# Kernel tuning notes

Measured on AMD Instinct MI355X. Metric: run time of the kernel, lower is better.

## Reference

```python
import jax, jax.numpy as jnp
import numpy as np

# pywt 'db4' decomposition filters (8 taps)
DEC_LO = np.array([-0.010597401784997278, 0.032883011666982945, 0.030841381835986965,
                   -0.18703481171888114, -0.02798376941698385, 0.6308807679295904,
                   0.7148465705525415, 0.23037781330885523], dtype=np.float32)
DEC_HI = np.array([-0.23037781330885523, 0.7148465705525415, -0.6308807679295904,
                   -0.02798376941698385, 0.18703481171888114, 0.030841381835986965,
                   -0.032883011666982945, -0.010597401784997278], dtype=np.float32)
FLEN = 8


def _dwt_last_axis(x, kern):
    """Single-level DWT along the last axis, pywt 'symmetric' mode.
    Equivalent to: pad symmetric by FLEN-1, np.convolve(ext, filt, 'valid')[1::2].
    kern: [2, 1, FLEN] (already time-reversed filters -> cross-correlation == convolution).
    Returns (lo, hi) each of shape x.shape[:-1] + (floor((n+FLEN-1)/2),).
    """
    pad = [(0, 0)] * (x.ndim - 1) + [(FLEN - 1, FLEN - 1)]
    xp = jnp.pad(x, pad, mode='symmetric')[..., 1:]  # drop 1 -> stride-2 grid starts at offset 1
    lead = xp.shape[:-1]
    xr = xp.reshape(-1, 1, xp.shape[-1])             # [N, 1, Lp]
    y = jax.lax.conv_general_dilated(
        xr, kern, window_strides=(2,), padding='VALID',
        dimension_numbers=('NCH', 'OIH', 'NCH'))     # [N, 2, out]
    y = y.reshape(lead + (2, y.shape[-1]))
    return y[..., 0, :], y[..., 1, :]


def setup_inputs() -> dict:
    key = jax.random.key(0)
    x = jax.random.normal(key, (8, 32, 512, 512), dtype=jnp.float32)
    return {"x": x}


def reference(x):
    # Batched 2D db4 DWT (pywt.dwt2, mode='symmetric') over [B, C, H, W].
    kern = jnp.stack([jnp.asarray(DEC_LO)[::-1], jnp.asarray(DEC_HI)[::-1]])[:, None, :]  # [2,1,8]
    # filter along W (axis -1)
    a_w, d_w = _dwt_last_axis(x, kern)
    # filter along H (axis -2): swap H/W, filter last axis, swap back
    def along_h(t):
        lo, hi = _dwt_last_axis(jnp.swapaxes(t, -1, -2), kern)
        return jnp.swapaxes(lo, -1, -2), jnp.swapaxes(hi, -1, -2)
    LL, LH = along_h(a_w)   # LL = aa, LH = cH = 'da' (detail along H, approx along W)
    HL, HH = along_h(d_w)   # HL = cV = 'ad', HH = cD = 'dd'
    return jnp.stack([LL, LH, HL, HH])  # [4, B, C, Ho, Wo]
```

## Files before the change

### kernel.cpp

```cpp
#include <hip/hip_runtime.h>


namespace {

constexpr int N   = 512;
constexpr int HO  = 259;
constexpr int NBC = 256;
constexpr int TOH = 12;
constexpr int NS  = (HO + TOH - 1) / TOH;
constexpr int NCG = 65;

typedef float f4 __attribute__((ext_vector_type(4)));
typedef f4 __attribute__((aligned(4))) f4u;
typedef float f2 __attribute__((ext_vector_type(2)));
typedef f2 __attribute__((aligned(4))) f2u;

__device__ constexpr float GL[8] = {
     0.23037781330885523f,  0.7148465705525415f,   0.6308807679295904f,
    -0.02798376941698385f, -0.18703481171888114f,  0.030841381835986965f,
     0.032883011666982945f,-0.010597401784997278f};
__device__ constexpr float GH[8] = {
    -0.010597401784997278f,-0.032883011666982945f, 0.030841381835986965f,
     0.18703481171888114f, -0.02798376941698385f, -0.6308807679295904f,
     0.7148465705525415f,  -0.23037781330885523f};

__device__ constexpr int LMAP[14] = {5,4,3,2,1,0,0,1,2,3,4,5,6,7};
__device__ constexpr int RMAP[14] = {8,9,10,11,12,13,13,12,11,10,9,8,7,6};

__device__ __forceinline__ int ext_idx(int j) {
    int v = j - 7;
    v = (j < 7)     ? (6 - j)         : v;
    v = (j > N + 6) ? (2 * N + 6 - j) : v;
    return v;
}

__device__ __forceinline__ void hconv(const float* __restrict__ base, int mode,
                                      f4& lo, f4& hi) {
    const f4 a = *(const f4u*)(base);
    const f4 b = *(const f4u*)(base + 4);
    const f4 c = *(const f4u*)(base + 8);
    const f2 d = *(const f2u*)(base + 12);
    const float win[14] = {a.x,a.y,a.z,a.w, b.x,b.y,b.z,b.w,
                           c.x,c.y,c.z,c.w, d.x,d.y};
    float v[14];
    if (mode == 0) {
        #pragma unroll
        for (int f = 0; f < 14; ++f) v[f] = win[f];
    } else if (mode < 0) {
        #pragma unroll
        for (int f = 0; f < 14; ++f) v[f] = win[LMAP[f]];
    } else {
        #pragma unroll
        for (int f = 0; f < 14; ++f) v[f] = win[RMAP[f]];
    }
    #pragma unroll
    for (int o = 0; o < 4; ++o) {
        float l = 0.f, h = 0.f;
        #pragma unroll
        for (int k = 0; k < 8; ++k) {
            l = fmaf(v[2 * o + k], GL[k], l);
            h = fmaf(v[2 * o + k], GH[k], h);
        }
        lo[o] = l; hi[o] = h;
    }
}

__global__ __launch_bounds__(256)
void dwt2_db4_reg(const float* __restrict__ x, float* __restrict__ out) {
    const int id   = blockIdx.x * 256 + threadIdx.x;
    const int cg   = id % NCG;
    const int rest = id / NCG;
    const int st   = rest % NS;
    const int bc   = rest / NS;
    const int c0   = 4 * cg;
    const int g0   = 2 * c0 - 6;
    const int g0c  = min(max(g0, 0), N - 14);
    const int mode = (cg == 0) ? -1 : ((cg == NCG - 1) ? 1 : 0);
    const float* __restrict__ img = x + (size_t)bc * (N * N);
    const int eh0 = 2 * (st * TOH) + 1;

    f4 rlo[8], rhi[8];
    #pragma unroll
    for (int r = 0; r < 6; ++r)
        hconv(img + (size_t)ext_idx(eh0 + r) * N + g0c, mode, rlo[r], rhi[r]);

    const size_t sub = (size_t)NBC * HO * HO;
    float* __restrict__ obase = out + (size_t)bc * (HO * HO);

#define STEP(U) do {                                                          \
    const int uo_ = ob * 4 + (U);                                             \
    const int e_  = eh0 + 2 * uo_ + 6;                                        \
    hconv(img + (size_t)ext_idx(e_)     * N + g0c, mode,                      \
          rlo[(6 + 2 * (U)) & 7], rhi[(6 + 2 * (U)) & 7]);                    \
    hconv(img + (size_t)ext_idx(e_ + 1) * N + g0c, mode,                      \
          rlo[(7 + 2 * (U)) & 7], rhi[(7 + 2 * (U)) & 7]);                    \
    f4 ll = {0,0,0,0}, lh = {0,0,0,0}, hl = {0,0,0,0}, hh = {0,0,0,0};        \
    _Pragma("unroll")                                                         \
    for (int k = 0; k < 8; ++k) {                                             \
        const f4 a_ = rlo[(2 * (U) + k) & 7];                                 \
        const f4 d_ = rhi[(2 * (U) + k) & 7];                                 \
        const float gl = GL[k], gh = GH[k];                                   \
        ll.x = fmaf(a_.x, gl, ll.x); ll.y = fmaf(a_.y, gl, ll.y);             \
        ll.z = fmaf(a_.z, gl, ll.z); ll.w = fmaf(a_.w, gl, ll.w);             \
        lh.x = fmaf(a_.x, gh, lh.x); lh.y = fmaf(a_.y, gh, lh.y);             \
        lh.z = fmaf(a_.z, gh, lh.z); lh.w = fmaf(a_.w, gh, lh.w);             \
        hl.x = fmaf(d_.x, gl, hl.x); hl.y = fmaf(d_.y, gl, hl.y);             \
        hl.z = fmaf(d_.z, gl, hl.z); hl.w = fmaf(d_.w, gl, hl.w);             \
        hh.x = fmaf(d_.x, gh, hh.x); hh.y = fmaf(d_.y, gh, hh.y);             \
        hh.z = fmaf(d_.z, gh, hh.z); hh.w = fmaf(d_.w, gh, hh.w);             \
    }                                                                         \
    const int ho_ = st * TOH + uo_;                                           \
    if (ho_ < HO) {                                                           \
        const size_t p = (size_t)ho_ * HO + c0;                               \
        if (cg != NCG - 1) {                                                  \
            *(f4u*)(obase + p)           = ll;                                \
            *(f4u*)(obase + sub + p)     = lh;                                \
            *(f4u*)(obase + 2 * sub + p) = hl;                                \
            *(f4u*)(obase + 3 * sub + p) = hh;                                \
        } else {                                                              \
            _Pragma("unroll")                                                 \
            for (int o = 0; o < 3; ++o) {                                     \
                obase[p + o]           = ll[o];                               \
                obase[sub + p + o]     = lh[o];                               \
                obase[2 * sub + p + o] = hl[o];                               \
                obase[3 * sub + p + o] = hh[o];                               \
            }                                                                 \
        }                                                                     \
    }                                                                         \
} while (0)

    for (int ob = 0; ob < TOH / 4; ++ob) {
        STEP(0); STEP(1); STEP(2); STEP(3);
    }
#undef STEP
}

}

extern "C" void kernel_launch(void* const* d_in, const int* in_sizes, int n_in,
                              void* d_out, int out_size, void* d_ws, size_t ws_size,
                              hipStream_t stream) {
    const float* x = (const float*)d_in[0];
    float* out = (float*)d_out;
    const int items  = NBC * NS * NCG;
    const int blocks = items / 256;
    dwt2_db4_reg<<<blocks, 256, 0, stream>>>(x, out);
}
```

Before: 143.8 us.

## Halve per-thread column work and use aligned 16-byte horizontal window loads

Each thread now computes two output columns instead of four, doubling the thread count, and loads a 12-float window from a 16-byte-aligned base with aligned vector loads instead of an unaligned 14-float window. Boundary handling is expanded to four symmetric-extension modes for the first two and last two column groups. This aims to raise parallelism, lower register pressure and use aligned loads. In exchange, redundant horizontal reads grow and output stores shrink to 8 bytes.

```diff
diff --git a/kernel.cpp b/kernel.cpp
--- a/kernel.cpp
+++ b/kernel.cpp
@@ -7,11 +7,10 @@
 constexpr int HO  = 259;
 constexpr int NBC = 256;
 constexpr int TOH = 12;
-constexpr int NS  = (HO + TOH - 1) / TOH;
-constexpr int NCG = 65;
+constexpr int NS  = 22;
+constexpr int NCG = 130;
 
 typedef float f4 __attribute__((ext_vector_type(4)));
-typedef f4 __attribute__((aligned(4))) f4u;
 typedef float f2 __attribute__((ext_vector_type(2)));
 typedef f2 __attribute__((aligned(4))) f2u;
 
@@ -24,10 +23,13 @@
      0.18703481171888114f, -0.02798376941698385f, -0.6308807679295904f,
      0.7148465705525415f,  -0.23037781330885523f};
 
-__device__ constexpr int LMAP[14] = {5,4,3,2,1,0,0,1,2,3,4,5,6,7};
-__device__ constexpr int RMAP[14] = {8,9,10,11,12,13,13,12,11,10,9,8,7,6};
+__device__ constexpr int IMAP[10] = {2,3,4,5,6,7,8,9,10,11};
+__device__ constexpr int LM0[10] = {5,4,3,2,1,0,0,1,2,3};
+__device__ constexpr int LM1[10] = {1,0,0,1,2,3,4,5,6,7};
+__device__ constexpr int RM0[10] = {6,7,8,9,10,11,11,10,9,8};
+__device__ constexpr int RM1[10] = {10,11,11,10,9,8,7,6,5,4};
 
-__device__ __forceinline__ int ext_idx(int j) {
+__device__ __forceinline__ int ext_row(int j) {
     int v = j - 7;
     v = (j < 7)     ? (6 - j)         : v;
     v = (j > N + 6) ? (2 * N + 6 - j) : v;
@@ -35,26 +37,36 @@
 }
 
 __device__ __forceinline__ void hconv(const float* __restrict__ base, int mode,
-                                      f4& lo, f4& hi) {
-    const f4 a = *(const f4u*)(base);
-    const f4 b = *(const f4u*)(base + 4);
-    const f4 c = *(const f4u*)(base + 8);
-    const f2 d = *(const f2u*)(base + 12);
-    const float win[14] = {a.x,a.y,a.z,a.w, b.x,b.y,b.z,b.w,
-                           c.x,c.y,c.z,c.w, d.x,d.y};
-    float v[14];
-    if (mode == 0) {
+                                      f2& lo, f2& hi) {
+    const f4 a = *(const f4*)(base);
+    const f4 b = *(const f4*)(base + 4);
+    const f4 c = *(const f4*)(base + 8);
+    const float win[12] = {a.x,a.y,a.z,a.w, b.x,b.y,b.z,b.w, c.x,c.y,c.z,c.w};
+    float v[10];
+    switch (mode) {
+    case 0:
         #pragma unroll
-        for (int f = 0; f < 14; ++f) v[f] = win[f];
-    } else if (mode < 0) {
+        for (int f = 0; f < 10; ++f) v[f] = win[IMAP[f]];
+        break;
+    case 1:
         #pragma unroll
-        for (int f = 0; f < 14; ++f) v[f] = win[LMAP[f]];
-    } else {
+        for (int f = 0; f < 10; ++f) v[f] = win[LM0[f]];
+        break;
+    case 2:
         #pragma unroll
-        for (int f = 0; f < 14; ++f) v[f] = win[RMAP[f]];
+        for (int f = 0; f < 10; ++f) v[f] = win[LM1[f]];
+        break;
+    case 3:
+        #pragma unroll
+        for (int f = 0; f < 10; ++f) v[f] = win[RM0[f]];
+        break;
+    default:
+        #pragma unroll
+        for (int f = 0; f < 10; ++f) v[f] = win[RM1[f]];
+        break;
     }
     #pragma unroll
-    for (int o = 0; o < 4; ++o) {
+    for (int o = 0; o < 2; ++o) {
         float l = 0.f, h = 0.f;
         #pragma unroll
         for (int k = 0; k < 8; ++k) {
@@ -66,23 +78,23 @@
 }
 
 __global__ __launch_bounds__(256)
-void dwt2_db4_reg(const float* __restrict__ x, float* __restrict__ out) {
+void dwt2_db4_reg2(const float* __restrict__ x, float* __restrict__ out) {
     const int id   = blockIdx.x * 256 + threadIdx.x;
     const int cg   = id % NCG;
     const int rest = id / NCG;
     const int st   = rest % NS;
     const int bc   = rest / NS;
-    const int c0   = 4 * cg;
-    const int g0   = 2 * c0 - 6;
-    const int g0c  = min(max(g0, 0), N - 14);
-    const int mode = (cg == 0) ? -1 : ((cg == NCG - 1) ? 1 : 0);
+    const int c0   = 2 * cg;
+    const int gb   = min(max(4 * cg - 8, 0), N - 12);
+    const int mode = (cg == 0) ? 1 : (cg == 1) ? 2 :
+                     (cg == NCG - 2) ? 3 : (cg == NCG - 1) ? 4 : 0;
     const float* __restrict__ img = x + (size_t)bc * (N * N);
     const int eh0 = 2 * (st * TOH) + 1;
 
-    f4 rlo[8], rhi[8];
+    f2 rlo[8], rhi[8];
     #pragma unroll
     for (int r = 0; r < 6; ++r)
-        hconv(img + (size_t)ext_idx(eh0 + r) * N + g0c, mode, rlo[r], rhi[r]);
+        hconv(img + (size_t)ext_row(eh0 + r) * N + gb, mode, rlo[r], rhi[r]);
 
     const size_t sub = (size_t)NBC * HO * HO;
     float* __restrict__ obase = out + (size_t)bc * (HO * HO);
@@ -90,41 +102,34 @@
 #define STEP(U) do {                                                          \
     const int uo_ = ob * 4 + (U);                                             \
     const int e_  = eh0 + 2 * uo_ + 6;                                        \
-    hconv(img + (size_t)ext_idx(e_)     * N + g0c, mode,                      \
+    hconv(img + (size_t)ext_row(e_)     * N + gb, mode,                       \
           rlo[(6 + 2 * (U)) & 7], rhi[(6 + 2 * (U)) & 7]);                    \
-    hconv(img + (size_t)ext_idx(e_ + 1) * N + g0c, mode,                      \
+    hconv(img + (size_t)ext_row(e_ + 1) * N + gb, mode,                       \
           rlo[(7 + 2 * (U)) & 7], rhi[(7 + 2 * (U)) & 7]);                    \
-    f4 ll = {0,0,0,0}, lh = {0,0,0,0}, hl = {0,0,0,0}, hh = {0,0,0,0};        \
+    f2 ll = {0,0}, lh = {0,0}, hl = {0,0}, hh = {0,0};                        \
     _Pragma("unroll")                                                         \
     for (int k = 0; k < 8; ++k) {                                             \
-        const f4 a_ = rlo[(2 * (U) + k) & 7];                                 \
-        const f4 d_ = rhi[(2 * (U) + k) & 7];                                 \
+        const f2 a_ = rlo[(2 * (U) + k) & 7];                                 \
+        const f2 d_ = rhi[(2 * (U) + k) & 7];                                 \
         const float gl = GL[k], gh = GH[k];                                   \
         ll.x = fmaf(a_.x, gl, ll.x); ll.y = fmaf(a_.y, gl, ll.y);             \
-        ll.z = fmaf(a_.z, gl, ll.z); ll.w = fmaf(a_.w, gl, ll.w);             \
         lh.x = fmaf(a_.x, gh, lh.x); lh.y = fmaf(a_.y, gh, lh.y);             \
-        lh.z = fmaf(a_.z, gh, lh.z); lh.w = fmaf(a_.w, gh, lh.w);             \
         hl.x = fmaf(d_.x, gl, hl.x); hl.y = fmaf(d_.y, gl, hl.y);             \
-        hl.z = fmaf(d_.z, gl, hl.z); hl.w = fmaf(d_.w, gl, hl.w);             \
         hh.x = fmaf(d_.x, gh, hh.x); hh.y = fmaf(d_.y, gh, hh.y);             \
-        hh.z = fmaf(d_.z, gh, hh.z); hh.w = fmaf(d_.w, gh, hh.w);             \
     }                                                                         \
     const int ho_ = st * TOH + uo_;                                           \
     if (ho_ < HO) {                                                           \
         const size_t p = (size_t)ho_ * HO + c0;                               \
         if (cg != NCG - 1) {                                                  \
-            *(f4u*)(obase + p)           = ll;                                \
-            *(f4u*)(obase + sub + p)     = lh;                                \
-            *(f4u*)(obase + 2 * sub + p) = hl;                                \
-            *(f4u*)(obase + 3 * sub + p) = hh;                                \
+            *(f2u*)(obase + p)           = ll;                                \
+            *(f2u*)(obase + sub + p)     = lh;                                \
+            *(f2u*)(obase + 2 * sub + p) = hl;                                \
+            *(f2u*)(obase + 3 * sub + p) = hh;                                \
         } else {                                                              \
-            _Pragma("unroll")                                                 \
-            for (int o = 0; o < 3; ++o) {                                     \
-                obase[p + o]           = ll[o];                               \
-                obase[sub + p + o]     = lh[o];                               \
-                obase[2 * sub + p + o] = hl[o];                               \
-                obase[3 * sub + p + o] = hh[o];                               \
-            }                                                                 \
+            obase[p]           = ll.x;                                        \
+            obase[sub + p]     = lh.x;                                        \
+            obase[2 * sub + p] = hl.x;                                        \
+            obase[3 * sub + p] = hh.x;                                        \
         }                                                                     \
     }                                                                         \
 } while (0)
@@ -144,5 +149,5 @@
     float* out = (float*)d_out;
     const int items  = NBC * NS * NCG;
     const int blocks = items / 256;
-    dwt2_db4_reg<<<blocks, 256, 0, stream>>>(x, out);
+    dwt2_db4_reg2<<<blocks, 256, 0, stream>>>(x, out);
 }
```

Result: slower. 153.4 us (+6.7%).

## Stream rows with scatter accumulation, aligned 16-float loads and row prefetch

Applied to the files above, without the earlier changes.

Replaces the ring buffer of horizontally filtered rows with a streaming scheme. Each input row is horizontally convolved once, then scattered into four rotating output accumulators; each output row is stored as soon as its last contributing input row is consumed. Row loads now use a 16-byte aligned 16-float window with one-row-ahead prefetch (double-buffered registers), replacing the unaligned 14-float loads. It relies on the fully unrolled 30-row schedule to keep the accumulator indices static, at some register cost.

```diff
diff --git a/kernel.cpp b/kernel.cpp
--- a/kernel.cpp
+++ b/kernel.cpp
@@ -3,17 +3,16 @@
 
 namespace {
 
-constexpr int N   = 512;
-constexpr int HO  = 259;
-constexpr int NBC = 256;
-constexpr int TOH = 12;
-constexpr int NS  = (HO + TOH - 1) / TOH;
-constexpr int NCG = 65;
+constexpr int N    = 512;
+constexpr int HO   = 259;
+constexpr int NBC  = 256;
+constexpr int TOH  = 12;
+constexpr int NS   = 22;
+constexpr int NCG  = 65;
+constexpr int MIDR = 2 * TOH + 6;
 
 typedef float f4 __attribute__((ext_vector_type(4)));
 typedef f4 __attribute__((aligned(4))) f4u;
-typedef float f2 __attribute__((ext_vector_type(2)));
-typedef f2 __attribute__((aligned(4))) f2u;
 
 __device__ constexpr float GL[8] = {
      0.23037781330885523f,  0.7148465705525415f,   0.6308807679295904f,
@@ -25,27 +24,23 @@
      0.7148465705525415f,  -0.23037781330885523f};
 
 __device__ constexpr int LMAP[14] = {5,4,3,2,1,0,0,1,2,3,4,5,6,7};
-__device__ constexpr int RMAP[14] = {8,9,10,11,12,13,13,12,11,10,9,8,7,6};
+__device__ constexpr int RMAP[14] = {10,11,12,13,14,15,15,14,13,12,11,10,9,8};
 
-__device__ __forceinline__ int ext_idx(int j) {
+__device__ __forceinline__ int ext_row(int j) {
     int v = j - 7;
     v = (j < 7)     ? (6 - j)         : v;
     v = (j > N + 6) ? (2 * N + 6 - j) : v;
     return v;
 }
 
-__device__ __forceinline__ void hconv(const float* __restrict__ base, int mode,
-                                      f4& lo, f4& hi) {
-    const f4 a = *(const f4u*)(base);
-    const f4 b = *(const f4u*)(base + 4);
-    const f4 c = *(const f4u*)(base + 8);
-    const f2 d = *(const f2u*)(base + 12);
-    const float win[14] = {a.x,a.y,a.z,a.w, b.x,b.y,b.z,b.w,
-                           c.x,c.y,c.z,c.w, d.x,d.y};
+__device__ __forceinline__ void hconv16(const f4& A, const f4& B, const f4& C,
+                                        const f4& D, int mode, f4& lo, f4& hi) {
+    const float win[16] = {A.x,A.y,A.z,A.w, B.x,B.y,B.z,B.w,
+                           C.x,C.y,C.z,C.w, D.x,D.y,D.z,D.w};
     float v[14];
     if (mode == 0) {
         #pragma unroll
-        for (int f = 0; f < 14; ++f) v[f] = win[f];
+        for (int f = 0; f < 14; ++f) v[f] = win[2 + f];
     } else if (mode < 0) {
         #pragma unroll
         for (int f = 0; f < 14; ++f) v[f] = win[LMAP[f]];
@@ -66,73 +61,99 @@
 }
 
 __global__ __launch_bounds__(256)
-void dwt2_db4_reg(const float* __restrict__ x, float* __restrict__ out) {
+void dwt2_db4_stream(const float* __restrict__ x, float* __restrict__ out) {
     const int id   = blockIdx.x * 256 + threadIdx.x;
     const int cg   = id % NCG;
     const int rest = id / NCG;
     const int st   = rest % NS;
     const int bc   = rest / NS;
     const int c0   = 4 * cg;
-    const int g0   = 2 * c0 - 6;
-    const int g0c  = min(max(g0, 0), N - 14);
+    const int ab   = min(max(8 * cg - 8, 0), N - 16);
     const int mode = (cg == 0) ? -1 : ((cg == NCG - 1) ? 1 : 0);
     const float* __restrict__ img = x + (size_t)bc * (N * N);
     const int eh0 = 2 * (st * TOH) + 1;
-
-    f4 rlo[8], rhi[8];
-    #pragma unroll
-    for (int r = 0; r < 6; ++r)
-        hconv(img + (size_t)ext_idx(eh0 + r) * N + g0c, mode, rlo[r], rhi[r]);
-
     const size_t sub = (size_t)NBC * HO * HO;
     float* __restrict__ obase = out + (size_t)bc * (HO * HO);
 
-#define STEP(U) do {                                                          \
-    const int uo_ = ob * 4 + (U);                                             \
-    const int e_  = eh0 + 2 * uo_ + 6;                                        \
-    hconv(img + (size_t)ext_idx(e_)     * N + g0c, mode,                      \
-          rlo[(6 + 2 * (U)) & 7], rhi[(6 + 2 * (U)) & 7]);                    \
-    hconv(img + (size_t)ext_idx(e_ + 1) * N + g0c, mode,                      \
-          rlo[(7 + 2 * (U)) & 7], rhi[(7 + 2 * (U)) & 7]);                    \
-    f4 ll = {0,0,0,0}, lh = {0,0,0,0}, hl = {0,0,0,0}, hh = {0,0,0,0};        \
-    _Pragma("unroll")                                                         \
-    for (int k = 0; k < 8; ++k) {                                             \
-        const f4 a_ = rlo[(2 * (U) + k) & 7];                                 \
-        const f4 d_ = rhi[(2 * (U) + k) & 7];                                 \
-        const float gl = GL[k], gh = GH[k];                                   \
-        ll.x = fmaf(a_.x, gl, ll.x); ll.y = fmaf(a_.y, gl, ll.y);             \
-        ll.z = fmaf(a_.z, gl, ll.z); ll.w = fmaf(a_.w, gl, ll.w);             \
-        lh.x = fmaf(a_.x, gh, lh.x); lh.y = fmaf(a_.y, gh, lh.y);             \
-        lh.z = fmaf(a_.z, gh, lh.z); lh.w = fmaf(a_.w, gh, lh.w);             \
-        hl.x = fmaf(d_.x, gl, hl.x); hl.y = fmaf(d_.y, gl, hl.y);             \
-        hl.z = fmaf(d_.z, gl, hl.z); hl.w = fmaf(d_.w, gl, hl.w);             \
-        hh.x = fmaf(d_.x, gh, hh.x); hh.y = fmaf(d_.y, gh, hh.y);             \
-        hh.z = fmaf(d_.z, gh, hh.z); hh.w = fmaf(d_.w, gh, hh.w);             \
-    }                                                                         \
-    const int ho_ = st * TOH + uo_;                                           \
-    if (ho_ < HO) {                                                           \
-        const size_t p = (size_t)ho_ * HO + c0;                               \
-        if (cg != NCG - 1) {                                                  \
-            *(f4u*)(obase + p)           = ll;                                \
-            *(f4u*)(obase + sub + p)     = lh;                                \
-            *(f4u*)(obase + 2 * sub + p) = hl;                                \
-            *(f4u*)(obase + 3 * sub + p) = hh;                                \
-        } else {                                                              \
-            _Pragma("unroll")                                                 \
-            for (int o = 0; o < 3; ++o) {                                     \
-                obase[p + o]           = ll[o];                               \
-                obase[sub + p + o]     = lh[o];                               \
-                obase[2 * sub + p + o] = hl[o];                               \
-                obase[3 * sub + p + o] = hh[o];                               \
+    f4 P[4][4];
+    #pragma unroll
+    for (int s = 0; s < 4; ++s)
+        #pragma unroll
+        for (int q = 0; q < 4; ++q) P[s][q] = (f4){0.f, 0.f, 0.f, 0.f};
+
+    f4 b0a, b0b, b0c, b0d, b1a, b1b, b1c, b1d;
+
+#define PRE(rn_, A_, B_, C_, D_) do {                                         \
+    const float* rp_ = img + (size_t)ext_row(eh0 + (rn_)) * N + ab;           \
+    A_ = *(const f4*)(rp_);      B_ = *(const f4*)(rp_ + 4);                  \
+    C_ = *(const f4*)(rp_ + 8);  D_ = *(const f4*)(rp_ + 12);                 \
+} while (0)
+
+#define UPD(r_, uo_) do { if ((uo_) >= 0 && (uo_) < TOH) {                    \
+    const int kk_ = (r_) - 2 * (uo_);                                         \
+    const int sl_ = (uo_) & 3;                                                \
+    const float gl_ = GL[kk_], gh_ = GH[kk_];                                 \
+    P[sl_][0] += lo * gl_;  P[sl_][1] += lo * gh_;                            \
+    P[sl_][2] += hi * gl_;  P[sl_][3] += hi * gh_;                            \
+} } while (0)
+
+#define FIN(r_) do {                                                          \
+    const int uo_ = ((r_) - 7) / 2;                                           \
+    if (uo_ >= 0 && uo_ < TOH) {                                              \
+        const int sl_ = uo_ & 3;                                              \
+        const int ho_ = st * TOH + uo_;                                       \
+        if (ho_ < HO) {                                                       \
+            const size_t p_ = (size_t)ho_ * HO + c0;                          \
+            if (cg != NCG - 1) {                                              \
+                *(f4u*)(obase + p_)           = P[sl_][0];                    \
+                *(f4u*)(obase + sub + p_)     = P[sl_][1];                    \
+                *(f4u*)(obase + 2 * sub + p_) = P[sl_][2];                    \
+                *(f4u*)(obase + 3 * sub + p_) = P[sl_][3];                    \
+            } else {                                                          \
+                _Pragma("unroll")                                             \
+                for (int o = 0; o < 3; ++o) {                                 \
+                    obase[p_ + o]           = P[sl_][0][o];                   \
+                    obase[sub + p_ + o]     = P[sl_][1][o];                   \
+                    obase[2 * sub + p_ + o] = P[sl_][2][o];                   \
+                    obase[3 * sub + p_ + o] = P[sl_][3][o];                   \
+                }                                                             \
             }                                                                 \
         }                                                                     \
+        P[sl_][0] = (f4){0.f,0.f,0.f,0.f};  P[sl_][1] = (f4){0.f,0.f,0.f,0.f};\
+        P[sl_][2] = (f4){0.f,0.f,0.f,0.f};  P[sl_][3] = (f4){0.f,0.f,0.f,0.f};\
     }                                                                         \
 } while (0)
 
-    for (int ob = 0; ob < TOH / 4; ++ob) {
-        STEP(0); STEP(1); STEP(2); STEP(3);
-    }
-#undef STEP
+#define ROW(r_, CA_, CB_, CC_, CD_, NA_, NB_, NC_, ND_) do {                  \
+    if ((r_) + 1 < MIDR) PRE((r_) + 1, NA_, NB_, NC_, ND_);                   \
+    f4 lo, hi;                                                                \
+    hconv16(CA_, CB_, CC_, CD_, mode, lo, hi);                                \
+    if (((r_) & 1) == 0) {                                                    \
+        UPD(r_, (r_) / 2);     UPD(r_, (r_) / 2 - 1);                         \
+        UPD(r_, (r_) / 2 - 2); UPD(r_, (r_) / 2 - 3);                         \
+    } else {                                                                  \
+        UPD(r_, ((r_) - 1) / 2); UPD(r_, ((r_) - 3) / 2);                     \
+        UPD(r_, ((r_) - 5) / 2); UPD(r_, ((r_) - 7) / 2);                     \
+        FIN(r_);                                                              \
+    }                                                                         \
+} while (0)
+
+#define ROW_E(r_) ROW(r_, b0a,b0b,b0c,b0d, b1a,b1b,b1c,b1d)
+#define ROW_O(r_) ROW(r_, b1a,b1b,b1c,b1d, b0a,b0b,b0c,b0d)
+
+    PRE(0, b0a, b0b, b0c, b0d);
+    ROW_E(0);  ROW_O(1);  ROW_E(2);  ROW_O(3);  ROW_E(4);  ROW_O(5);
+    ROW_E(6);  ROW_O(7);  ROW_E(8);  ROW_O(9);  ROW_E(10); ROW_O(11);
+    ROW_E(12); ROW_O(13); ROW_E(14); ROW_O(15); ROW_E(16); ROW_O(17);
+    ROW_E(18); ROW_O(19); ROW_E(20); ROW_O(21); ROW_E(22); ROW_O(23);
+    ROW_E(24); ROW_O(25); ROW_E(26); ROW_O(27); ROW_E(28); ROW_O(29);
+
+#undef ROW_E
+#undef ROW_O
+#undef ROW
+#undef FIN
+#undef UPD
+#undef PRE
 }
 
 }
@@ -144,5 +165,5 @@
     float* out = (float*)d_out;
     const int items  = NBC * NS * NCG;
     const int blocks = items / 256;
-    dwt2_db4_reg<<<blocks, 256, 0, stream>>>(x, out);
+    dwt2_db4_stream<<<blocks, 256, 0, stream>>>(x, out);
 }
```

New measurement: 136.6 us. -5.1%, faster.
